# Kernel optimization log

Measured on AMD Instinct MI355X. Metric: run time of the kernel, lower is better.

The kernel has to match this reference:

```python
import jax, jax.numpy as jnp
import numpy as np

N = 10000    # nodes
D = 128      # d_model
K = 16       # d_state
S = 5        # seq_len (tokens per node)
E = 320000   # edges
R = 200      # num relation types
P = E // (S - 1)  # edges sampled per tokenizer step
EPS = 1e-5


def setup_inputs() -> dict:
    key = jax.random.key(0)
    ks = jax.random.split(key, 16)
    sc = 1.0 / np.sqrt(D)
    return {
        "x": jax.random.normal(ks[0], (N, D), jnp.float32),
        "edge_index": jax.random.randint(ks[1], (2, E), 0, N),
        "edge_type": jax.random.randint(ks[2], (E,), 0, R),
        "perms": jax.random.randint(ks[3], (S - 1, P), 0, E),
        "rel_table": jax.random.normal(ks[4], (R, D), jnp.float32) * 0.1,
        "log_A": jax.random.normal(ks[5], (D, K), jnp.float32) * 0.1,
        "W_B": jax.random.normal(ks[6], (D, K), jnp.float32) * sc,
        "W_C": jax.random.normal(ks[7], (D, K), jnp.float32) * sc,
        "W_delta": jax.random.normal(ks[8], (D, D), jnp.float32) * sc,
        "b_delta": jnp.zeros((D,), jnp.float32),
        "W_g": jax.random.normal(ks[9], (D, D), jnp.float32) * sc,
        "b_g": jnp.zeros((D,), jnp.float32),
        "W_out": jax.random.normal(ks[10], (D, D), jnp.float32) * sc,
        "b_out": jnp.zeros((D,), jnp.float32),
        "ln_g": jnp.ones((D,), jnp.float32),
        "ln_b": jnp.zeros((D,), jnp.float32),
    }


def _tokenize(x, edge_index, edge_type, perms, rel_table):
    # x: [N,D]; perms: [S-1,P] -> tokens [N,S,D]
    src, dst = edge_index[0], edge_index[1]
    step_src = src[perms]                    # [S-1,P]
    step_dst = dst[perms]                    # [S-1,P]
    msg = x[step_src] + rel_table[edge_type[perms]]  # [S-1,P,D]
    seg = jax.vmap(lambda i, m: jax.ops.segment_sum(m, i, num_segments=N))(step_dst, msg)  # [S-1,N,D]
    deg = jax.vmap(lambda i: jax.ops.segment_sum(jnp.ones((P,), x.dtype), i, num_segments=N))(step_dst)  # [S-1,N]
    neigh = seg / jnp.clip(deg, 1.0)[..., None]
    return jnp.concatenate([x[:, None, :], jnp.moveaxis(neigh, 0, 1)], axis=1)  # [N,S,D]


def _selective_scan(tokens, log_A, W_B, W_C, W_delta, b_delta):
    # tokens: [N,S,D] -> [N,S,D]
    deltas = jax.nn.softplus(tokens @ W_delta + b_delta)  # [N,S,D]
    Bs = tokens @ W_B                                     # [N,S,K]
    Cs = tokens @ W_C                                     # [N,S,K]
    A_cont = -jnp.exp(log_A)                              # [D,K]
    A_disc = jnp.exp(deltas[..., None] * A_cont)          # [N,S,D,K]
    Bx = deltas[..., None] * Bs[:, :, None, :] * tokens[..., None]  # [N,S,D,K] = B_disc * x_k

    def step(state, xs):
        a, bx, c = xs                          # [N,D,K],[N,D,K],[N,K]
        state = a * state + bx
        y = jnp.einsum('ndk,nk->nd', state, c)
        return state, y

    init = jnp.zeros((tokens.shape[0], D, K), tokens.dtype)
    _, ys = jax.lax.scan(step, init, (jnp.moveaxis(A_disc, 1, 0),
                                      jnp.moveaxis(Bx, 1, 0),
                                      jnp.moveaxis(Cs, 1, 0)))
    return jnp.moveaxis(ys, 0, 1)  # [N,S,D]


def reference(x, edge_index, edge_type, perms, rel_table, log_A, W_B, W_C,
              W_delta, b_delta, W_g, b_g, W_out, b_out, ln_g, ln_b):
    tokens = _tokenize(x, edge_index, edge_type, perms, rel_table)
    out_f = _selective_scan(tokens, log_A, W_B, W_C, W_delta, b_delta)
    out_b = _selective_scan(tokens[:, ::-1, :], log_A, W_B, W_C, W_delta, b_delta)
    scan_out = (out_f + out_b[:, ::-1, :]).mean(axis=1)  # [N,D]
    gate = jax.nn.silu(x @ W_g + b_g)
    res = x + gate * (scan_out @ W_out + b_out)
    mu = res.mean(axis=-1, keepdims=True)
    var = res.var(axis=-1, keepdims=True)
    return (res - mu) / jnp.sqrt(var + EPS) * ln_g + ln_b
```

## Files before the change

kernel.cpp:

```cpp
#include <hip/hip_runtime.h>
#include <hip/hip_bf16.h>
#include <math.h>

#define N_NODES 10000
#define D_MODEL 128
#define E_EDGES 320000
#define P_EDGES 80000
#define LN_EPS 1e-5f
#define NBUCK 40960
#define CAP 32
#define M_ROWS 50000
#define M_PAD  50048
#define NCOLS 160

typedef __attribute__((ext_vector_type(8))) short bf16x8;
typedef __attribute__((ext_vector_type(4))) float f32x4;

__device__ __forceinline__ unsigned short f2bf(float f) {
    __hip_bfloat16 h = __float2bfloat16(f);
    return *reinterpret_cast<unsigned short*>(&h);
}
__device__ __forceinline__ float bf2f(unsigned int u) {
    return __uint_as_float(u << 16);
}

__global__ __launch_bounds__(256) void prep_all(
    const float* __restrict__ Wd, const float* __restrict__ Wb,
    const float* __restrict__ Wc, const float* __restrict__ Wg,
    const float* __restrict__ W_out,
    const float* __restrict__ x, const float* __restrict__ rel,
    const int* __restrict__ edge_index, const int* __restrict__ edge_type,
    unsigned short* __restrict__ Bp, unsigned short* __restrict__ Wop,
    unsigned short* __restrict__ Wgp,
    unsigned short* __restrict__ x_bf, unsigned short* __restrict__ rel_bf,
    int* __restrict__ cnt, int4* __restrict__ ed4,
    unsigned short* __restrict__ tokens)
{
    int gid = blockIdx.x * 256 + threadIdx.x;
    if (gid < 20480) {
        int k = gid / NCOLS, n = gid - (gid / NCOLS) * NCOLS;
        float v;
        if (n < 128)      v = Wd[k * 128 + n];
        else if (n < 144) v = Wb[k * 16 + (n - 128)];
        else              v = Wc[k * 16 + (n - 144)];
        Bp[((size_t)(k >> 3) * NCOLS + n) * 8 + (k & 7)] = f2bf(v);
    } else if (gid < 36864) {
        int i = gid - 20480;
        int k = i >> 7, n = i & 127;
        Wop[((size_t)(k >> 3) * 128 + n) * 8 + (k & 7)] = f2bf(W_out[k * 128 + n]);
    } else if (gid < 53248) {
        int i = gid - 36864;
        int k = i >> 7, n = i & 127;
        Wgp[((size_t)(k >> 3) * 128 + n) * 8 + (k & 7)] = f2bf(Wg[k * 128 + n]);
    } else if (gid < 94208) {
        cnt[gid - 53248] = 0;
    } else if (gid < 119808) {
        int i = gid - 94208;
        rel_bf[i] = f2bf(rel[i]);
    } else if (gid < 1399808) {
        int i = gid - 119808;
        unsigned short v = f2bf(x[i]);
        x_bf[i] = v;
        tokens[(size_t)(i >> 7) * 640 + (i & 127)] = v;
    } else if (gid < 1719808) {
        int e = gid - 1399808;
        ed4[e] = make_int4(edge_index[e], edge_index[E_EDGES + e], edge_type[e], 0);
    }
}

__global__ __launch_bounds__(256) void csr_build(
    const int4* __restrict__ ed4, const int* __restrict__ perms,
    int* __restrict__ cnt, int2* __restrict__ slots)
{
    int gid = blockIdx.x * blockDim.x + threadIdx.x;
    if (gid >= 4 * P_EDGES) return;
    int s = gid / P_EDGES;
    int e = perms[gid];
    int4 ed = ed4[e];
    int b = ed.y * 4 + s;
    int pos = atomicAdd(&cnt[b], 1);
    if (pos < CAP) slots[(size_t)b * CAP + pos] = make_int2(ed.x, ed.z);
}

__global__ __launch_bounds__(256) void gather_tokens(
    const unsigned short* __restrict__ x_bf,
    const int* __restrict__ cnt, const int2* __restrict__ slots,
    const unsigned short* __restrict__ rel_bf,
    unsigned short* __restrict__ tokens)
{
    int n = blockIdx.x;
    int w = threadIdx.x >> 6, lane = threadIdx.x & 63;
    int b = n * 4 + w;
    int c = cnt[b];
    int cc = c < CAP ? c : CAP;
    const int2* sl = slots + (size_t)b * CAP;
    const unsigned int* xu = (const unsigned int*)x_bf;
    const unsigned int* ru = (const unsigned int*)rel_bf;
    float ax = 0.f, ay = 0.f;
    int j = 0;
    for (; j + 4 <= cc; j += 4) {
        int4 e01 = *(const int4*)(sl + j);
        int4 e23 = *(const int4*)(sl + j + 2);
        unsigned int x0 = xu[(size_t)e01.x * 64 + lane];
        unsigned int r0 = ru[(size_t)e01.y * 64 + lane];
        unsigned int x1 = xu[(size_t)e01.z * 64 + lane];
        unsigned int r1 = ru[(size_t)e01.w * 64 + lane];
        unsigned int x2 = xu[(size_t)e23.x * 64 + lane];
        unsigned int r2 = ru[(size_t)e23.y * 64 + lane];
        unsigned int x3 = xu[(size_t)e23.z * 64 + lane];
        unsigned int r3 = ru[(size_t)e23.w * 64 + lane];
        ax += (bf2f(x0 & 0xffffu) + bf2f(r0 & 0xffffu))
            + (bf2f(x1 & 0xffffu) + bf2f(r1 & 0xffffu))
            + (bf2f(x2 & 0xffffu) + bf2f(r2 & 0xffffu))
            + (bf2f(x3 & 0xffffu) + bf2f(r3 & 0xffffu));
        ay += (bf2f(x0 >> 16) + bf2f(r0 >> 16))
            + (bf2f(x1 >> 16) + bf2f(r1 >> 16))
            + (bf2f(x2 >> 16) + bf2f(r2 >> 16))
            + (bf2f(x3 >> 16) + bf2f(r3 >> 16));
    }
    if (j + 2 <= cc) {
        int4 e01 = *(const int4*)(sl + j);
        unsigned int x0 = xu[(size_t)e01.x * 64 + lane];
        unsigned int r0 = ru[(size_t)e01.y * 64 + lane];
        unsigned int x1 = xu[(size_t)e01.z * 64 + lane];
        unsigned int r1 = ru[(size_t)e01.w * 64 + lane];
        ax += (bf2f(x0 & 0xffffu) + bf2f(r0 & 0xffffu))
            + (bf2f(x1 & 0xffffu) + bf2f(r1 & 0xffffu));
        ay += (bf2f(x0 >> 16) + bf2f(r0 >> 16))
            + (bf2f(x1 >> 16) + bf2f(r1 >> 16));
        j += 2;
    }
    if (j < cc) {
        int2 se = sl[j];
        unsigned int xa = xu[(size_t)se.x * 64 + lane];
        unsigned int ra = ru[(size_t)se.y * 64 + lane];
        ax += bf2f(xa & 0xffffu) + bf2f(ra & 0xffffu);
        ay += bf2f(xa >> 16) + bf2f(ra >> 16);
    }
    float inv = 1.f / fmaxf((float)c, 1.f);
    unsigned int pack = (unsigned int)f2bf(ax * inv)
                      | ((unsigned int)f2bf(ay * inv) << 16);
    ((unsigned int*)tokens)[((size_t)n * 5 + w + 1) * 64 + lane] = pack;
}

__global__ __launch_bounds__(256) void mfma_gemm(
    const unsigned short* __restrict__ tokens,
    const unsigned short* __restrict__ Bp,
    const float* __restrict__ b_delta,
    unsigned short* __restrict__ delta,
    unsigned short* __restrict__ bc)
{
    int m0 = blockIdx.x * 64;
    int wv = threadIdx.x >> 6, lane = threadIdx.x & 63;
    int quad = lane >> 4, l16 = lane & 15;

    f32x4 acc[10];
    #pragma unroll
    for (int t = 0; t < 10; ++t) acc[t] = (f32x4){0.f, 0.f, 0.f, 0.f};

    const unsigned short* arow = tokens + (size_t)(m0 + wv * 16 + l16) * 128 + quad * 8;
    #pragma unroll
    for (int kc = 0; kc < 128; kc += 32) {
        bf16x8 a = *(const bf16x8*)(arow + kc);
        #pragma unroll
        for (int t = 0; t < 10; ++t) {
            bf16x8 b = *(const bf16x8*)(Bp + ((size_t)(kc / 8 + quad) * NCOLS + 16 * t + l16) * 8);
            acc[t] = __builtin_amdgcn_mfma_f32_16x16x32_bf16(a, b, acc[t], 0, 0, 0);
        }
    }

    int rbase = m0 + wv * 16 + quad * 4;
    #pragma unroll
    for (int t = 0; t < 10; ++t) {
        int c = 16 * t + l16;
        #pragma unroll
        for (int reg = 0; reg < 4; ++reg) {
            int r = rbase + reg;
            if (r >= M_ROWS) continue;
            float v = acc[t][reg];
            if (t < 8) {
                float z = v + b_delta[c];
                float d = (z > 15.f) ? z : log1pf(__expf(z));
                delta[(size_t)r * 128 + c] = f2bf(d);
            } else {
                bc[(size_t)r * 32 + (c - 128)] = f2bf(v);
            }
        }
    }
}

__global__ __launch_bounds__(128) void scan_so(
    const unsigned short* __restrict__ tokens,
    const unsigned short* __restrict__ delta,
    const unsigned short* __restrict__ bcbuf,
    const float* __restrict__ log_A,
    unsigned short* __restrict__ so)
{
    const int n = blockIdx.x, t = threadIdx.x;
    __shared__ __align__(16) float BC[160];

    for (int idx = t; idx < 160; idx += 128)
        BC[idx] = bf2f(bcbuf[(size_t)n * 160 + idx]);

    float tv[5], dl[5];
    {
        const unsigned short* tb = tokens + (size_t)n * 640 + t;
        const unsigned short* db = delta  + (size_t)n * 640 + t;
        #pragma unroll
        for (int s = 0; s < 5; ++s) {
            tv[s] = bf2f(tb[s * 128]);
            dl[s] = bf2f(db[s * 128]);
        }
    }
    float Ac[16];
    {
        const float4* la = (const float4*)(log_A + t * 16);
        #pragma unroll
        for (int q = 0; q < 4; ++q) {
            float4 lv = la[q];
            Ac[q * 4 + 0] = -__expf(lv.x);
            Ac[q * 4 + 1] = -__expf(lv.y);
            Ac[q * 4 + 2] = -__expf(lv.z);
            Ac[q * 4 + 3] = -__expf(lv.w);
        }
    }
    __syncthreads();

    float st[16], V[16];
    #pragma unroll
    for (int k = 0; k < 16; ++k) { st[k] = 0.f; V[k] = BC[16 + k]; }
    float total = 0.f;
    #pragma unroll
    for (int s = 0; s < 5; ++s) {
        float dtv = dl[s] * tv[s];
        float yf = 0.f, ub = 0.f;
        #pragma unroll
        for (int k = 0; k < 16; ++k) {
            float B = BC[s * 32 + k];
            float C = BC[s * 32 + 16 + k];
            float A = __expf(dl[s] * Ac[k]);
            st[k] = fmaf(A, st[k], dtv * B);
            yf = fmaf(st[k], C, yf);
            ub = fmaf(V[k], B, ub);
            if (s < 4) V[k] = fmaf(A, V[k], BC[(s + 1) * 32 + 16 + k]);
        }
        total += yf + dtv * ub;
    }
    so[(size_t)n * 128 + t] = f2bf(total * 0.2f);
}

__global__ __launch_bounds__(256) void out_gemm(
    const unsigned short* __restrict__ so,
    const unsigned short* __restrict__ Wop,
    const unsigned short* __restrict__ Wgp,
    const unsigned short* __restrict__ x_bf,
    const float* __restrict__ x,
    const float* __restrict__ b_out, const float* __restrict__ b_g,
    const float* __restrict__ ln_g, const float* __restrict__ ln_b,
    float* __restrict__ out)
{
    int m0 = blockIdx.x * 16;
    int tid = threadIdx.x;
    int wv = tid >> 6, lane = tid & 63;
    int quad = lane >> 4, l16 = lane & 15;

    __shared__ float res[16 * 132];
    __shared__ float pmu[16][16];
    __shared__ float pv2[16][16];
    __shared__ float muA[16], rstdA[16];

    f32x4 accO[2] = {{0,0,0,0},{0,0,0,0}};
    f32x4 accG[2] = {{0,0,0,0},{0,0,0,0}};
    const unsigned short* arow = so   + (size_t)(m0 + l16) * 128 + quad * 8;
    const unsigned short* grow = x_bf + (size_t)(m0 + l16) * 128 + quad * 8;
    #pragma unroll
    for (int kc = 0; kc < 128; kc += 32) {
        bf16x8 a  = *(const bf16x8*)(arow + kc);
        bf16x8 ag = *(const bf16x8*)(grow + kc);
        #pragma unroll
        for (int tt = 0; tt < 2; ++tt) {
            int t = wv * 2 + tt;
            size_t bi = ((size_t)(kc / 8 + quad) * 128 + 16 * t + l16) * 8;
            bf16x8 bo = *(const bf16x8*)(Wop + bi);
            bf16x8 bg = *(const bf16x8*)(Wgp + bi);
            accO[tt] = __builtin_amdgcn_mfma_f32_16x16x32_bf16(a,  bo, accO[tt], 0, 0, 0);
            accG[tt] = __builtin_amdgcn_mfma_f32_16x16x32_bf16(ag, bg, accG[tt], 0, 0, 0);
        }
    }

    #pragma unroll
    for (int tt = 0; tt < 2; ++tt) {
        int c = wv * 32 + tt * 16 + l16;
        #pragma unroll
        for (int reg = 0; reg < 4; ++reg) {
            int lrow = quad * 4 + reg;
            int r = m0 + lrow;
            float o  = accO[tt][reg] + b_out[c];
            float gl = accG[tt][reg] + b_g[c];
            float gate = gl / (1.f + __expf(-gl));
            res[lrow * 132 + c] = x[(size_t)r * 128 + c] + gate * o;
        }
    }
    __syncthreads();

    {
        int row = tid >> 4, q = tid & 15;
        float s = 0.f, s2 = 0.f;
        #pragma unroll
        for (int i = 0; i < 8; ++i) {
            float v = res[row * 132 + q + 16 * i];
            s += v; s2 += v * v;
        }
        pmu[row][q] = s; pv2[row][q] = s2;
    }
    __syncthreads();
    if (tid < 16) {
        float s = 0.f, s2 = 0.f;
        #pragma unroll
        for (int i = 0; i < 16; ++i) { s += pmu[tid][i]; s2 += pv2[tid][i]; }
        float mu = s * (1.f / 128.f);
        float var = s2 * (1.f / 128.f) - mu * mu;
        muA[tid] = mu;
        rstdA[tid] = rsqrtf(var + LN_EPS);
    }
    __syncthreads();
    #pragma unroll
    for (int i = 0; i < 8; ++i) {
        int idx = i * 256 + tid;
        int row = idx >> 7, c = idx & 127;
        out[(size_t)(m0 + row) * 128 + c] =
            (res[row * 132 + c] - muA[row]) * rstdA[row] * ln_g[c] + ln_b[c];
    }
}

extern "C" void kernel_launch(void* const* d_in, const int* in_sizes, int n_in,
                              void* d_out, int out_size, void* d_ws, size_t ws_size,
                              hipStream_t stream) {
    const float* x          = (const float*)d_in[0];
    const int*   edge_index = (const int*)  d_in[1];
    const int*   edge_type  = (const int*)  d_in[2];
    const int*   perms      = (const int*)  d_in[3];
    const float* rel_table  = (const float*)d_in[4];
    const float* log_A      = (const float*)d_in[5];
    const float* W_B        = (const float*)d_in[6];
    const float* W_C        = (const float*)d_in[7];
    const float* W_delta    = (const float*)d_in[8];
    const float* b_delta    = (const float*)d_in[9];
    const float* W_g        = (const float*)d_in[10];
    const float* b_g        = (const float*)d_in[11];
    const float* W_out      = (const float*)d_in[12];
    const float* b_out      = (const float*)d_in[13];
    const float* ln_g       = (const float*)d_in[14];
    const float* ln_b       = (const float*)d_in[15];

    char* ws = (char*)d_ws;
    int*            cnt    = (int*)           (ws + 0);
    unsigned short* Bp     = (unsigned short*)(ws + 163840);
    unsigned short* Wop    = (unsigned short*)(ws + 204800);
    unsigned short* Wgp    = (unsigned short*)(ws + 237568);
    unsigned short* x_bf   = (unsigned short*)(ws + 270336);
    unsigned short* rel_bf = (unsigned short*)(ws + 2830336);
    int4*           ed4    = (int4*)          (ws + 2881536);
    unsigned short* tokens = (unsigned short*)(ws + 8001536);
    unsigned short* bc     = (unsigned short*)(ws + 20813824);
    int2*           slots  = (int2*)          (ws + 24013824);
    unsigned short* delta  = (unsigned short*)(ws + 24013824);
    unsigned short* so     = (unsigned short*)(ws + 36826112);

    prep_all<<<6718, 256, 0, stream>>>(
        W_delta, W_B, W_C, W_g, W_out, x, rel_table, edge_index, edge_type,
        Bp, Wop, Wgp, x_bf, rel_bf, cnt, ed4, tokens);

    csr_build<<<(4 * P_EDGES + 255) / 256, 256, 0, stream>>>(
        ed4, perms, cnt, slots);

    gather_tokens<<<N_NODES, 256, 0, stream>>>(
        x_bf, cnt, slots, rel_bf, tokens);

    mfma_gemm<<<M_PAD / 64, 256, 0, stream>>>(
        tokens, Bp, b_delta, delta, bc);

    scan_so<<<N_NODES, 128, 0, stream>>>(
        tokens, delta, bc, log_A, so);

    out_gemm<<<N_NODES / 16, 256, 0, stream>>>(
        so, Wop, Wgp, x_bf, x, b_out, b_g, ln_g, ln_b, (float*)d_out);
}
```

Baseline: 206.6 us.

## Fuse projection GEMM, selective scan and output GEMM into one kernel

```diff
diff --git a/kernel.cpp b/kernel.cpp
--- a/kernel.cpp
+++ b/kernel.cpp
@@ -7,10 +7,8 @@
 #define E_EDGES 320000
 #define P_EDGES 80000
 #define LN_EPS 1e-5f
-#define NBUCK 40960
 #define CAP 32
 #define M_ROWS 50000
-#define M_PAD  50048
 #define NCOLS 160
 
 typedef __attribute__((ext_vector_type(8))) short bf16x8;
@@ -143,193 +141,181 @@
     ((unsigned int*)tokens)[((size_t)n * 5 + w + 1) * 64 + lane] = pack;
 }
 
-__global__ __launch_bounds__(256) void mfma_gemm(
+__global__ __launch_bounds__(256) void mega(
     const unsigned short* __restrict__ tokens,
     const unsigned short* __restrict__ Bp,
-    const float* __restrict__ b_delta,
-    unsigned short* __restrict__ delta,
-    unsigned short* __restrict__ bc)
-{
-    int m0 = blockIdx.x * 64;
-    int wv = threadIdx.x >> 6, lane = threadIdx.x & 63;
-    int quad = lane >> 4, l16 = lane & 15;
-
-    f32x4 acc[10];
-    #pragma unroll
-    for (int t = 0; t < 10; ++t) acc[t] = (f32x4){0.f, 0.f, 0.f, 0.f};
-
-    const unsigned short* arow = tokens + (size_t)(m0 + wv * 16 + l16) * 128 + quad * 8;
-    #pragma unroll
-    for (int kc = 0; kc < 128; kc += 32) {
-        bf16x8 a = *(const bf16x8*)(arow + kc);
-        #pragma unroll
-        for (int t = 0; t < 10; ++t) {
-            bf16x8 b = *(const bf16x8*)(Bp + ((size_t)(kc / 8 + quad) * NCOLS + 16 * t + l16) * 8);
-            acc[t] = __builtin_amdgcn_mfma_f32_16x16x32_bf16(a, b, acc[t], 0, 0, 0);
-        }
-    }
-
-    int rbase = m0 + wv * 16 + quad * 4;
-    #pragma unroll
-    for (int t = 0; t < 10; ++t) {
-        int c = 16 * t + l16;
-        #pragma unroll
-        for (int reg = 0; reg < 4; ++reg) {
-            int r = rbase + reg;
-            if (r >= M_ROWS) continue;
-            float v = acc[t][reg];
-            if (t < 8) {
-                float z = v + b_delta[c];
-                float d = (z > 15.f) ? z : log1pf(__expf(z));
-                delta[(size_t)r * 128 + c] = f2bf(d);
-            } else {
-                bc[(size_t)r * 32 + (c - 128)] = f2bf(v);
-            }
-        }
-    }
-}
-
-__global__ __launch_bounds__(128) void scan_so(
-    const unsigned short* __restrict__ tokens,
-    const unsigned short* __restrict__ delta,
-    const unsigned short* __restrict__ bcbuf,
-    const float* __restrict__ log_A,
-    unsigned short* __restrict__ so)
-{
-    const int n = blockIdx.x, t = threadIdx.x;
-    __shared__ __align__(16) float BC[160];
-
-    for (int idx = t; idx < 160; idx += 128)
-        BC[idx] = bf2f(bcbuf[(size_t)n * 160 + idx]);
-
-    float tv[5], dl[5];
-    {
-        const unsigned short* tb = tokens + (size_t)n * 640 + t;
-        const unsigned short* db = delta  + (size_t)n * 640 + t;
-        #pragma unroll
-        for (int s = 0; s < 5; ++s) {
-            tv[s] = bf2f(tb[s * 128]);
-            dl[s] = bf2f(db[s * 128]);
-        }
-    }
-    float Ac[16];
-    {
-        const float4* la = (const float4*)(log_A + t * 16);
-        #pragma unroll
-        for (int q = 0; q < 4; ++q) {
-            float4 lv = la[q];
-            Ac[q * 4 + 0] = -__expf(lv.x);
-            Ac[q * 4 + 1] = -__expf(lv.y);
-            Ac[q * 4 + 2] = -__expf(lv.z);
-            Ac[q * 4 + 3] = -__expf(lv.w);
-        }
-    }
-    __syncthreads();
-
-    float st[16], V[16];
-    #pragma unroll
-    for (int k = 0; k < 16; ++k) { st[k] = 0.f; V[k] = BC[16 + k]; }
-    float total = 0.f;
-    #pragma unroll
-    for (int s = 0; s < 5; ++s) {
-        float dtv = dl[s] * tv[s];
-        float yf = 0.f, ub = 0.f;
-        #pragma unroll
-        for (int k = 0; k < 16; ++k) {
-            float B = BC[s * 32 + k];
-            float C = BC[s * 32 + 16 + k];
-            float A = __expf(dl[s] * Ac[k]);
-            st[k] = fmaf(A, st[k], dtv * B);
-            yf = fmaf(st[k], C, yf);
-            ub = fmaf(V[k], B, ub);
-            if (s < 4) V[k] = fmaf(A, V[k], BC[(s + 1) * 32 + 16 + k]);
-        }
-        total += yf + dtv * ub;
-    }
-    so[(size_t)n * 128 + t] = f2bf(total * 0.2f);
-}
-
-__global__ __launch_bounds__(256) void out_gemm(
-    const unsigned short* __restrict__ so,
     const unsigned short* __restrict__ Wop,
     const unsigned short* __restrict__ Wgp,
     const unsigned short* __restrict__ x_bf,
     const float* __restrict__ x,
-    const float* __restrict__ b_out, const float* __restrict__ b_g,
+    const float* __restrict__ log_A,
+    const float* __restrict__ b_delta, const float* __restrict__ b_g,
+    const float* __restrict__ b_out,
     const float* __restrict__ ln_g, const float* __restrict__ ln_b,
     float* __restrict__ out)
 {
-    int m0 = blockIdx.x * 16;
-    int tid = threadIdx.x;
-    int wv = tid >> 6, lane = tid & 63;
-    int quad = lane >> 4, l16 = lane & 15;
-
-    __shared__ float res[16 * 132];
-    __shared__ float pmu[16][16];
-    __shared__ float pv2[16][16];
-    __shared__ float muA[16], rstdA[16];
-
-    f32x4 accO[2] = {{0,0,0,0},{0,0,0,0}};
-    f32x4 accG[2] = {{0,0,0,0},{0,0,0,0}};
-    const unsigned short* arow = so   + (size_t)(m0 + l16) * 128 + quad * 8;
-    const unsigned short* grow = x_bf + (size_t)(m0 + l16) * 128 + quad * 8;
-    #pragma unroll
-    for (int kc = 0; kc < 128; kc += 32) {
-        bf16x8 a  = *(const bf16x8*)(arow + kc);
-        bf16x8 ag = *(const bf16x8*)(grow + kc);
+    const int tid = threadIdx.x;
+    const int wv = tid >> 6, lane = tid & 63;
+    const int quad = lane >> 4, l16 = lane & 15;
+    const int m0 = blockIdx.x * 80;
+    const int n0 = blockIdx.x * 16;
+
+    __shared__ __align__(16) char smem[34816];
+    unsigned short* s_delta = (unsigned short*)smem;
+    float*          s_bcf   = (float*)(smem + 20480);
+    unsigned short* s_so    = (unsigned short*)(smem + 30720);
+    float* s_res  = (float*)smem;
+    float* s_pmu  = (float*)(smem + 20480);
+    float* s_pv2  = (float*)(smem + 21504);
+    float* s_mu   = (float*)(smem + 22528);
+    float* s_rstd = (float*)(smem + 22592);
+
+    for (int u = wv; u < 50; u += 4) {
+        int f = u / 10, t = u - (u / 10) * 10;
+        f32x4 acc = {0.f, 0.f, 0.f, 0.f};
+        const unsigned short* arow =
+            tokens + (size_t)(m0 + f * 16 + l16) * 128 + quad * 8;
+        #pragma unroll
+        for (int kc = 0; kc < 128; kc += 32) {
+            bf16x8 a = *(const bf16x8*)(arow + kc);
+            bf16x8 b = *(const bf16x8*)(Bp +
+                ((size_t)(kc / 8 + quad) * NCOLS + 16 * t + l16) * 8);
+            acc = __builtin_amdgcn_mfma_f32_16x16x32_bf16(a, b, acc, 0, 0, 0);
+        }
+        int rbase = f * 16 + quad * 4;
+        int c = 16 * t + l16;
+        #pragma unroll
+        for (int reg = 0; reg < 4; ++reg) {
+            int r = rbase + reg;
+            float v = acc[reg];
+            if (t < 8) {
+                float z = v + b_delta[c];
+                float d = (z > 15.f) ? z : log1pf(__expf(z));
+                s_delta[r * 128 + c] = f2bf(d);
+            } else {
+                s_bcf[r * 32 + (c - 128)] = v;
+            }
+        }
+    }
+    __syncthreads();
+
+    {
+        const int dim = tid & 127;
+        float Ac[16];
+        {
+            const float4* la = (const float4*)(log_A + dim * 16);
+            #pragma unroll
+            for (int q = 0; q < 4; ++q) {
+                float4 lv = la[q];
+                Ac[q * 4 + 0] = -__expf(lv.x);
+                Ac[q * 4 + 1] = -__expf(lv.y);
+                Ac[q * 4 + 2] = -__expf(lv.z);
+                Ac[q * 4 + 3] = -__expf(lv.w);
+            }
+        }
+        #pragma unroll
+        for (int i = 0; i < 8; ++i) {
+            int node = (tid >> 7) + 2 * i;
+            const float* bcn = s_bcf + node * 160;
+            float tv[5], dl[5];
+            {
+                const unsigned short* tb =
+                    tokens + ((size_t)(n0 + node) * 5) * 128 + dim;
+                const unsigned short* db = s_delta + node * 640 + dim;
+                #pragma unroll
+                for (int s = 0; s < 5; ++s) {
+                    tv[s] = bf2f(tb[s * 128]);
+                    dl[s] = bf2f(db[s * 128]);
+                }
+            }
+            float st[16], V[16];
+            #pragma unroll
+            for (int k = 0; k < 16; ++k) { st[k] = 0.f; V[k] = bcn[16 + k]; }
+            float total = 0.f;
+            #pragma unroll
+            for (int s = 0; s < 5; ++s) {
+                float dtv = dl[s] * tv[s];
+                float yf = 0.f, ub = 0.f;
+                #pragma unroll
+                for (int k = 0; k < 16; ++k) {
+                    float B = bcn[s * 32 + k];
+                    float C = bcn[s * 32 + 16 + k];
+                    float A = __expf(dl[s] * Ac[k]);
+                    st[k] = fmaf(A, st[k], dtv * B);
+                    yf = fmaf(st[k], C, yf);
+                    ub = fmaf(V[k], B, ub);
+                    if (s < 4) V[k] = fmaf(A, V[k], bcn[(s + 1) * 32 + 16 + k]);
+                }
+                total += yf + dtv * ub;
+            }
+            s_so[node * 128 + (((dim >> 3) ^ (node & 7)) << 3) + (dim & 7)] =
+                f2bf(total * 0.2f);
+        }
+    }
+    __syncthreads();
+
+    {
+        f32x4 accO[2] = {{0,0,0,0},{0,0,0,0}};
+        f32x4 accG[2] = {{0,0,0,0},{0,0,0,0}};
+        const unsigned short* grow = x_bf + (size_t)(n0 + l16) * 128 + quad * 8;
+        #pragma unroll
+        for (int kc = 0; kc < 128; kc += 32) {
+            bf16x8 a = *(const bf16x8*)(s_so + l16 * 128 +
+                           (((kc / 8 + quad) ^ (l16 & 7)) << 3));
+            bf16x8 ag = *(const bf16x8*)(grow + kc);
+            #pragma unroll
+            for (int tt = 0; tt < 2; ++tt) {
+                int t = wv * 2 + tt;
+                size_t bi = ((size_t)(kc / 8 + quad) * 128 + 16 * t + l16) * 8;
+                bf16x8 bo = *(const bf16x8*)(Wop + bi);
+                bf16x8 bg = *(const bf16x8*)(Wgp + bi);
+                accO[tt] = __builtin_amdgcn_mfma_f32_16x16x32_bf16(a,  bo, accO[tt], 0, 0, 0);
+                accG[tt] = __builtin_amdgcn_mfma_f32_16x16x32_bf16(ag, bg, accG[tt], 0, 0, 0);
+            }
+        }
+
         #pragma unroll
         for (int tt = 0; tt < 2; ++tt) {
-            int t = wv * 2 + tt;
-            size_t bi = ((size_t)(kc / 8 + quad) * 128 + 16 * t + l16) * 8;
-            bf16x8 bo = *(const bf16x8*)(Wop + bi);
-            bf16x8 bg = *(const bf16x8*)(Wgp + bi);
-            accO[tt] = __builtin_amdgcn_mfma_f32_16x16x32_bf16(a,  bo, accO[tt], 0, 0, 0);
-            accG[tt] = __builtin_amdgcn_mfma_f32_16x16x32_bf16(ag, bg, accG[tt], 0, 0, 0);
-        }
-    }
-
-    #pragma unroll
-    for (int tt = 0; tt < 2; ++tt) {
-        int c = wv * 32 + tt * 16 + l16;
-        #pragma unroll
-        for (int reg = 0; reg < 4; ++reg) {
-            int lrow = quad * 4 + reg;
-            int r = m0 + lrow;
-            float o  = accO[tt][reg] + b_out[c];
-            float gl = accG[tt][reg] + b_g[c];
-            float gate = gl / (1.f + __expf(-gl));
-            res[lrow * 132 + c] = x[(size_t)r * 128 + c] + gate * o;
-        }
-    }
-    __syncthreads();
-
-    {
-        int row = tid >> 4, q = tid & 15;
-        float s = 0.f, s2 = 0.f;
+            int c = wv * 32 + tt * 16 + l16;
+            #pragma unroll
+            for (int reg = 0; reg < 4; ++reg) {
+                int lrow = quad * 4 + reg;
+                float o  = accO[tt][reg] + b_out[c];
+                float gl = accG[tt][reg] + b_g[c];
+                float gate = gl / (1.f + __expf(-gl));
+                s_res[lrow * 132 + c] = x[(size_t)(n0 + lrow) * 128 + c] + gate * o;
+            }
+        }
+        __syncthreads();
+
+        {
+            int row = tid >> 4, q = tid & 15;
+            float s = 0.f, s2 = 0.f;
+            #pragma unroll
+            for (int i = 0; i < 8; ++i) {
+                float vv = s_res[row * 132 + q + 16 * i];
+                s += vv; s2 += vv * vv;
+            }
+            s_pmu[row * 16 + q] = s; s_pv2[row * 16 + q] = s2;
+        }
+        __syncthreads();
+        if (tid < 16) {
+            float s = 0.f, s2 = 0.f;
+            #pragma unroll
+            for (int i = 0; i < 16; ++i) { s += s_pmu[tid * 16 + i]; s2 += s_pv2[tid * 16 + i]; }
+            float mu = s * (1.f / 128.f);
+            float var = s2 * (1.f / 128.f) - mu * mu;
+            s_mu[tid] = mu;
+            s_rstd[tid] = rsqrtf(var + LN_EPS);
+        }
+        __syncthreads();
         #pragma unroll
         for (int i = 0; i < 8; ++i) {
-            float v = res[row * 132 + q + 16 * i];
-            s += v; s2 += v * v;
-        }
-        pmu[row][q] = s; pv2[row][q] = s2;
-    }
-    __syncthreads();
-    if (tid < 16) {
-        float s = 0.f, s2 = 0.f;
-        #pragma unroll
-        for (int i = 0; i < 16; ++i) { s += pmu[tid][i]; s2 += pv2[tid][i]; }
-        float mu = s * (1.f / 128.f);
-        float var = s2 * (1.f / 128.f) - mu * mu;
-        muA[tid] = mu;
-        rstdA[tid] = rsqrtf(var + LN_EPS);
-    }
-    __syncthreads();
-    #pragma unroll
-    for (int i = 0; i < 8; ++i) {
-        int idx = i * 256 + tid;
-        int row = idx >> 7, c = idx & 127;
-        out[(size_t)(m0 + row) * 128 + c] =
-            (res[row * 132 + c] - muA[row]) * rstdA[row] * ln_g[c] + ln_b[c];
+            int idx = i * 256 + tid;
+            int row = idx >> 7, c = idx & 127;
+            out[(size_t)(n0 + row) * 128 + c] =
+                (s_res[row * 132 + c] - s_mu[row]) * s_rstd[row] * ln_g[c] + ln_b[c];
+        }
     }
 }
 
@@ -362,10 +348,7 @@
     unsigned short* rel_bf = (unsigned short*)(ws + 2830336);
     int4*           ed4    = (int4*)          (ws + 2881536);
     unsigned short* tokens = (unsigned short*)(ws + 8001536);
-    unsigned short* bc     = (unsigned short*)(ws + 20813824);
-    int2*           slots  = (int2*)          (ws + 24013824);
-    unsigned short* delta  = (unsigned short*)(ws + 24013824);
-    unsigned short* so     = (unsigned short*)(ws + 36826112);
+    int2*           slots  = (int2*)          (ws + 20801536);
 
     prep_all<<<6718, 256, 0, stream>>>(
         W_delta, W_B, W_C, W_g, W_out, x, rel_table, edge_index, edge_type,
@@ -377,12 +360,7 @@
     gather_tokens<<<N_NODES, 256, 0, stream>>>(
         x_bf, cnt, slots, rel_bf, tokens);
 
-    mfma_gemm<<<M_PAD / 64, 256, 0, stream>>>(
-        tokens, Bp, b_delta, delta, bc);
-
-    scan_so<<<N_NODES, 128, 0, stream>>>(
-        tokens, delta, bc, log_A, so);
-
-    out_gemm<<<N_NODES / 16, 256, 0, stream>>>(
-        so, Wop, Wgp, x_bf, x, b_out, b_g, ln_g, ln_b, (float*)d_out);
-}
+    mega<<<N_NODES / 16, 256, 0, stream>>>(
+        tokens, Bp, Wop, Wgp, x_bf, x, log_A, b_delta, b_g, b_out,
+        ln_g, ln_b, (float*)d_out);
+}
```

Result: no change. 207.2 us (+0.3%).
